# Kernel optimization log

Measured on AMD Instinct MI355X. Metric: run time of the kernel, lower is better.

The kernel has to match this reference:

```python
import jax, jax.numpy as jnp
import numpy as np

B, N, C = 4, 4096, 2048
EPS = 1e-5  # torch.nn.LayerNorm default


def setup_inputs() -> dict:
    key = jax.random.key(0)
    kx, = jax.random.split(key, 1)
    x = jax.random.normal(kx, (B, N, C), dtype=jnp.float32)
    gamma = jnp.ones((C,), dtype=jnp.float32)   # LayerNorm weight
    beta = jnp.zeros((C,), dtype=jnp.float32)   # LayerNorm bias
    return {"x": x, "gamma": gamma, "beta": beta}


def reference(x, gamma, beta):
    # The original repeats x to (B,N,N,C), applies a (no-op on the diagonal)
    # triu mask, FFTs every row over C, and extracts the (n,n) diagonal.
    # The diagonal rows are exactly the unmasked originals, so this equals:
    #   LayerNorm(real(fft(x, axis=-1)))
    y = jnp.fft.fft(x, axis=-1).real  # (B,N,C)
    mu = jnp.mean(y, axis=-1, keepdims=True)
    var = jnp.mean(jnp.square(y - mu), axis=-1, keepdims=True)  # biased, as torch LN
    return (y - mu) * jax.lax.rsqrt(var + EPS) * gamma + beta
```

## Files before the change

kernel.cpp:

```cpp
#include <hip/hip_runtime.h>
#include <math.h>


#define TPB 256
#define CD  2048

__device__ __forceinline__ float2 cadd(float2 a, float2 b){ return make_float2(a.x+b.x, a.y+b.y); }
__device__ __forceinline__ float2 csub(float2 a, float2 b){ return make_float2(a.x-b.x, a.y-b.y); }

__device__ __forceinline__ void dft8(const float2* z, float2* y)
{
    const float C8 = 0.70710678118654752440f;
    float2 a0=cadd(z[0],z[4]), a1=cadd(z[1],z[5]), a2=cadd(z[2],z[6]), a3=cadd(z[3],z[7]);
    float2 b0=csub(z[0],z[4]), b1=csub(z[1],z[5]), b2=csub(z[2],z[6]), b3=csub(z[3],z[7]);
    float2 t1=make_float2(C8*(b1.x+b1.y), C8*(b1.y-b1.x));
    float2 t2=make_float2(b2.y, -b2.x);
    float2 t3=make_float2(C8*(b3.y-b3.x), -C8*(b3.x+b3.y));
    {
        float pr=a0.x+a2.x, pi=a0.y+a2.y, mr=a0.x-a2.x, mi=a0.y-a2.y;
        float qr=a1.x+a3.x, qi=a1.y+a3.y, nr=a1.x-a3.x, ni=a1.y-a3.y;
        y[0]=make_float2(pr+qr,pi+qi); y[2]=make_float2(mr+ni,mi-nr);
        y[4]=make_float2(pr-qr,pi-qi); y[6]=make_float2(mr-ni,mi+nr);
    }
    {
        float pr=b0.x+t2.x, pi=b0.y+t2.y, mr=b0.x-t2.x, mi=b0.y-t2.y;
        float qr=t1.x+t3.x, qi=t1.y+t3.y, nr=t1.x-t3.x, ni=t1.y-t3.y;
        y[1]=make_float2(pr+qr,pi+qi); y[3]=make_float2(mr+ni,mi-nr);
        y[5]=make_float2(pr-qr,pi-qi); y[7]=make_float2(mr-ni,mi+nr);
    }
}

template<int S_, int OFFM>
__device__ __forceinline__ void r8_store(float2* Lw, const float2* y, int p)
{
    Lw[0] = y[0];
    if (S_ == 64 && p == 0) {
#pragma unroll
        for (int r = 1; r < 8; ++r) Lw[OFFM*r] = y[r];
        return;
    }
    const float th = -6.28318530717958647692f * ((float)S_ / 2048.0f);
    float s1, c1;
    __sincosf(th * (float)p, &s1, &c1);
    const float c2 = c1*c1 - s1*s1, s2 = 2.0f*c1*s1;
    const float c4 = c2*c2 - s2*s2, s4 = 2.0f*c2*s2;
    const float c3 = c1*c2 - s1*s2, s3 = s1*c2 + c1*s2;
    const float c5 = c1*c4 - s1*s4, s5 = s1*c4 + c1*s4;
    const float c6 = c2*c4 - s2*s4, s6 = s2*c4 + c2*s4;
    const float c7 = c3*c4 - s3*s4, s7 = s3*c4 + c3*s4;
    const float cw[8] = {1.f, c1, c2, c3, c4, c5, c6, c7};
    const float sw[8] = {0.f, s1, s2, s3, s4, s5, s6, s7};
#pragma unroll
    for (int r = 1; r < 8; ++r)
        Lw[OFFM*r] = make_float2(cw[r]*y[r].x - sw[r]*y[r].y,
                                 cw[r]*y[r].y + sw[r]*y[r].x);
}

__global__ __launch_bounds__(TPB, 8) void fourier_ln_kernel(
    const float* __restrict__ x,
    const float* __restrict__ gamma,
    const float* __restrict__ beta,
    float* __restrict__ out)
{
    __shared__ float2 L[2304];
    __shared__ float rmem[16];

    const int t  = threadIdx.x;
    const int t8 = t >> 3;
    const long long row0 = 2LL * (long long)blockIdx.x;
    const float* __restrict__ x0 = x + row0 * CD;
    const float* __restrict__ x1 = x0 + CD;

    float2 z[8], y[8];
#pragma unroll
    for (int r = 0; r < 8; ++r) {
        const int k = t + 256*r;
        z[r] = make_float2(x0[k], x1[k]);
    }

    float2* const Lr = L + (t + t8);

    dft8(z, y);
    r8_store<1, 1>(L + 9*t, y, t);
    __syncthreads();
#pragma unroll
    for (int r = 0; r < 8; ++r) z[r] = Lr[288*r];
    __syncthreads();

    dft8(z, y);
    r8_store<8, 9>(L + ((t & 7) + 72*t8), y, t8);
    __syncthreads();
#pragma unroll
    for (int r = 0; r < 8; ++r) z[r] = Lr[288*r];
    __syncthreads();

    dft8(z, y);
    {
        const int q = t & 63, p = t >> 6;
        r8_store<64, 72>(L + (q + (q >> 3) + 576*p), y, p);
    }
    __syncthreads();

    const int u   = t >> 1;
    const int sig = (t & 1) ? ((u == 0) ? 128 : 256 - u) : u;

    {
        const float2* Lsig = L + (sig + (sig >> 3));
#pragma unroll
        for (int r = 0; r < 8; ++r) z[r] = Lsig[288*r];
    }

    float gv[8], bv[8];
#pragma unroll
    for (int j = 0; j < 8; ++j) {
        gv[j] = gamma[sig + 256*j];
        bv[j] = beta[sig + 256*j];
    }

    float2 Z[8];
    {
        float pr=z[0].x+z[4].x, pi=z[0].y+z[4].y, mr=z[0].x-z[4].x, mi=z[0].y-z[4].y;
        float qr=z[2].x+z[6].x, qi=z[2].y+z[6].y, nr=z[2].x-z[6].x, ni=z[2].y-z[6].y;
        Z[0]=make_float2(pr+qr,pi+qi); Z[2]=make_float2(mr+ni,mi-nr);
        Z[4]=make_float2(pr-qr,pi-qi); Z[6]=make_float2(mr-ni,mi+nr);
    }
    {
        float pr=z[1].x+z[5].x, pi=z[1].y+z[5].y, mr=z[1].x-z[5].x, mi=z[1].y-z[5].y;
        float qr=z[3].x+z[7].x, qi=z[3].y+z[7].y, nr=z[3].x-z[7].x, ni=z[3].y-z[7].y;
        Z[1]=make_float2(pr+qr,pi+qi); Z[3]=make_float2(mr+ni,mi-nr);
        Z[5]=make_float2(pr-qr,pi-qi); Z[7]=make_float2(mr-ni,mi+nr);
    }

    float y0v[8], y1v[8];
    float s0=0.f, ss0=0.f, s1=0.f, ss1=0.f;
#pragma unroll
    for (int j = 0; j < 8; ++j) {
        float vx = __shfl_xor(Z[7-j].x, 1, 64);
        float vy = __shfl_xor(Z[7-j].y, 1, 64);
        const int ja = (8-j) & 7;
        float ax = (t == 0) ? Z[ja].x : Z[7-j].x;
        float ay = (t == 0) ? Z[ja].y : Z[7-j].y;
        vx = (t < 2) ? ax : vx;
        vy = (t < 2) ? ay : vy;
        float a = 0.5f*(Z[j].x + vx);
        float b = 0.5f*(Z[j].y + vy);
        y0v[j]=a; y1v[j]=b;
        s0+=a; ss0+=a*a; s1+=b; ss1+=b*b;
    }

#pragma unroll
    for (int off = 32; off > 0; off >>= 1) {
        s0  += __shfl_down(s0,  off, 64);
        ss0 += __shfl_down(ss0, off, 64);
        s1  += __shfl_down(s1,  off, 64);
        ss1 += __shfl_down(ss1, off, 64);
    }
    const int wave = t >> 6;
    if ((t & 63) == 0) {
        rmem[4*wave+0]=s0; rmem[4*wave+1]=ss0; rmem[4*wave+2]=s1; rmem[4*wave+3]=ss1;
    }
    __syncthreads();
    float S0=0.f, SS0=0.f, S1=0.f, SS1=0.f;
#pragma unroll
    for (int w = 0; w < 4; ++w) {
        S0+=rmem[4*w+0]; SS0+=rmem[4*w+1]; S1+=rmem[4*w+2]; SS1+=rmem[4*w+3];
    }
    const float inv = 1.0f/(float)CD;
    const float mu0 = S0*inv, mu1 = S1*inv;
    const float r0 = rsqrtf(SS0*inv - mu0*mu0 + 1e-5f);
    const float r1 = rsqrtf(SS1*inv - mu1*mu1 + 1e-5f);

    float* __restrict__ o0 = out + row0*CD;
    float* __restrict__ o1 = o0 + CD;
#pragma unroll
    for (int j = 0; j < 8; ++j) {
        const int k = sig + 256*j;
        const float rg0 = r0 * gv[j], rg1 = r1 * gv[j];
        o0[k] = (y0v[j] - mu0) * rg0 + bv[j];
        o1[k] = (y1v[j] - mu1) * rg1 + bv[j];
    }
}

extern "C" void kernel_launch(void* const* d_in, const int* in_sizes, int n_in,
                              void* d_out, int out_size, void* d_ws, size_t ws_size,
                              hipStream_t stream) {
    (void)in_sizes; (void)n_in; (void)d_ws; (void)ws_size; (void)out_size;
    const float* x     = (const float*)d_in[0];
    const float* gamma = (const float*)d_in[1];
    const float* beta  = (const float*)d_in[2];
    float* out = (float*)d_out;

    const int total_rows = 4 * 4096;
    const int blocks = total_rows / 2;
    fourier_ln_kernel<<<blocks, TPB, 0, stream>>>(x, gamma, beta, out);
}
```

Before: 236.9 us.

## Process four rows per block sharing twiddles and barriers across two FFT pairs

Each block now handles two packed complex row pairs (four real rows) with separate shared buffers, computing twiddle factors once per stage and reusing them for both pairs. This halves the number of barriers and twiddle sincos evaluations per row and gives more independent work between syncs. In exchange it doubles shared memory and register use per block and lowers the launch-bounds occupancy hint from 8 to 4 blocks, and halves the grid size.

```diff
diff --git a/kernel.cpp b/kernel.cpp
--- a/kernel.cpp
+++ b/kernel.cpp
@@ -30,93 +30,34 @@
     }
 }
 
-template<int S_, int OFFM>
-__device__ __forceinline__ void r8_store(float2* Lw, const float2* y, int p)
+__device__ __forceinline__ void make_tw(float th1, float* cw, float* sw)
+{
+    float s1, c1;
+    __sincosf(th1, &s1, &c1);
+    cw[0]=1.f;                       sw[0]=0.f;
+    cw[1]=c1;                        sw[1]=s1;
+    cw[2]=c1*c1-s1*s1;               sw[2]=2.f*c1*s1;
+    cw[4]=cw[2]*cw[2]-sw[2]*sw[2];   sw[4]=2.f*cw[2]*sw[2];
+    cw[3]=c1*cw[2]-s1*sw[2];         sw[3]=s1*cw[2]+c1*sw[2];
+    cw[5]=c1*cw[4]-s1*sw[4];         sw[5]=s1*cw[4]+c1*sw[4];
+    cw[6]=cw[2]*cw[4]-sw[2]*sw[4];   sw[6]=sw[2]*cw[4]+cw[2]*sw[4];
+    cw[7]=cw[3]*cw[4]-sw[3]*sw[4];   sw[7]=sw[3]*cw[4]+cw[3]*sw[4];
+}
+
+template<int OFFM>
+__device__ __forceinline__ void r8_store(float2* Lw, const float2* y,
+                                         const float* cw, const float* sw)
 {
     Lw[0] = y[0];
-    if (S_ == 64 && p == 0) {
-#pragma unroll
-        for (int r = 1; r < 8; ++r) Lw[OFFM*r] = y[r];
-        return;
-    }
-    const float th = -6.28318530717958647692f * ((float)S_ / 2048.0f);
-    float s1, c1;
-    __sincosf(th * (float)p, &s1, &c1);
-    const float c2 = c1*c1 - s1*s1, s2 = 2.0f*c1*s1;
-    const float c4 = c2*c2 - s2*s2, s4 = 2.0f*c2*s2;
-    const float c3 = c1*c2 - s1*s2, s3 = s1*c2 + c1*s2;
-    const float c5 = c1*c4 - s1*s4, s5 = s1*c4 + c1*s4;
-    const float c6 = c2*c4 - s2*s4, s6 = s2*c4 + c2*s4;
-    const float c7 = c3*c4 - s3*s4, s7 = s3*c4 + c3*s4;
-    const float cw[8] = {1.f, c1, c2, c3, c4, c5, c6, c7};
-    const float sw[8] = {0.f, s1, s2, s3, s4, s5, s6, s7};
 #pragma unroll
     for (int r = 1; r < 8; ++r)
         Lw[OFFM*r] = make_float2(cw[r]*y[r].x - sw[r]*y[r].y,
                                  cw[r]*y[r].y + sw[r]*y[r].x);
 }
 
-__global__ __launch_bounds__(TPB, 8) void fourier_ln_kernel(
-    const float* __restrict__ x,
-    const float* __restrict__ gamma,
-    const float* __restrict__ beta,
-    float* __restrict__ out)
-{
-    __shared__ float2 L[2304];
-    __shared__ float rmem[16];
-
-    const int t  = threadIdx.x;
-    const int t8 = t >> 3;
-    const long long row0 = 2LL * (long long)blockIdx.x;
-    const float* __restrict__ x0 = x + row0 * CD;
-    const float* __restrict__ x1 = x0 + CD;
-
-    float2 z[8], y[8];
-#pragma unroll
-    for (int r = 0; r < 8; ++r) {
-        const int k = t + 256*r;
-        z[r] = make_float2(x0[k], x1[k]);
-    }
-
-    float2* const Lr = L + (t + t8);
-
-    dft8(z, y);
-    r8_store<1, 1>(L + 9*t, y, t);
-    __syncthreads();
-#pragma unroll
-    for (int r = 0; r < 8; ++r) z[r] = Lr[288*r];
-    __syncthreads();
-
-    dft8(z, y);
-    r8_store<8, 9>(L + ((t & 7) + 72*t8), y, t8);
-    __syncthreads();
-#pragma unroll
-    for (int r = 0; r < 8; ++r) z[r] = Lr[288*r];
-    __syncthreads();
-
-    dft8(z, y);
-    {
-        const int q = t & 63, p = t >> 6;
-        r8_store<64, 72>(L + (q + (q >> 3) + 576*p), y, p);
-    }
-    __syncthreads();
-
-    const int u   = t >> 1;
-    const int sig = (t & 1) ? ((u == 0) ? 128 : 256 - u) : u;
-
-    {
-        const float2* Lsig = L + (sig + (sig >> 3));
-#pragma unroll
-        for (int r = 0; r < 8; ++r) z[r] = Lsig[288*r];
-    }
-
-    float gv[8], bv[8];
-#pragma unroll
-    for (int j = 0; j < 8; ++j) {
-        gv[j] = gamma[sig + 256*j];
-        bv[j] = beta[sig + 256*j];
-    }
-
+__device__ __forceinline__ void stageD_untangle(const float2* z, int t,
+        float* y0v, float* y1v, float& s0, float& ss0, float& s1, float& ss1)
+{
     float2 Z[8];
     {
         float pr=z[0].x+z[4].x, pi=z[0].y+z[4].y, mr=z[0].x-z[4].x, mi=z[0].y-z[4].y;
@@ -130,9 +71,6 @@
         Z[1]=make_float2(pr+qr,pi+qi); Z[3]=make_float2(mr+ni,mi-nr);
         Z[5]=make_float2(pr-qr,pi-qi); Z[7]=make_float2(mr-ni,mi+nr);
     }
-
-    float y0v[8], y1v[8];
-    float s0=0.f, ss0=0.f, s1=0.f, ss1=0.f;
 #pragma unroll
     for (int j = 0; j < 8; ++j) {
         float vx = __shfl_xor(Z[7-j].x, 1, 64);
@@ -147,37 +85,137 @@
         y0v[j]=a; y1v[j]=b;
         s0+=a; ss0+=a*a; s1+=b; ss1+=b*b;
     }
+}
+
+__global__ __launch_bounds__(TPB, 4) void fourier_ln_kernel(
+    const float* __restrict__ x,
+    const float* __restrict__ gamma,
+    const float* __restrict__ beta,
+    float* __restrict__ out)
+{
+    __shared__ float2 LA[2304];
+    __shared__ float2 LB[2304];
+    __shared__ float rmem[32];
+
+    const int t  = threadIdx.x;
+    const int t8 = t >> 3;
+    const long long rowa = 4LL * (long long)blockIdx.x;
+    const float* __restrict__ xa0 = x + rowa * CD;
+    const float* __restrict__ xa1 = xa0 + CD;
+    const float* __restrict__ xb0 = xa0 + 2 * CD;
+    const float* __restrict__ xb1 = xa0 + 3 * CD;
+
+    float2 za[8], zb[8], y[8];
+#pragma unroll
+    for (int r = 0; r < 8; ++r) {
+        const int k = t + 256*r;
+        za[r] = make_float2(xa0[k], xa1[k]);
+    }
+#pragma unroll
+    for (int r = 0; r < 8; ++r) {
+        const int k = t + 256*r;
+        zb[r] = make_float2(xb0[k], xb1[k]);
+    }
+
+    float2* const LAr = LA + (t + t8);
+    float2* const LBr = LB + (t + t8);
+
+    float cw[8], sw[8];
+
+    make_tw(-3.06796157577128245943e-3f * (float)t, cw, sw);
+    dft8(za, y);  r8_store<1>(LA + 9*t, y, cw, sw);
+    dft8(zb, y);  r8_store<1>(LB + 9*t, y, cw, sw);
+    __syncthreads();
+#pragma unroll
+    for (int r = 0; r < 8; ++r) za[r] = LAr[288*r];
+#pragma unroll
+    for (int r = 0; r < 8; ++r) zb[r] = LBr[288*r];
+    __syncthreads();
+
+    make_tw(-2.45436926061702596755e-2f * (float)t8, cw, sw);
+    dft8(za, y);  r8_store<9>(LA + ((t & 7) + 72*t8), y, cw, sw);
+    dft8(zb, y);  r8_store<9>(LB + ((t & 7) + 72*t8), y, cw, sw);
+    __syncthreads();
+#pragma unroll
+    for (int r = 0; r < 8; ++r) za[r] = LAr[288*r];
+#pragma unroll
+    for (int r = 0; r < 8; ++r) zb[r] = LBr[288*r];
+    __syncthreads();
+
+    {
+        const int q = t & 63, p = t >> 6;
+        make_tw(-1.96349540849362077404e-1f * (float)p, cw, sw);
+        const int off = q + (q >> 3) + 576*p;
+        dft8(za, y);  r8_store<72>(LA + off, y, cw, sw);
+        dft8(zb, y);  r8_store<72>(LB + off, y, cw, sw);
+    }
+    __syncthreads();
+
+    const int u   = t >> 1;
+    const int sig = (t & 1) ? ((u == 0) ? 128 : 256 - u) : u;
+
+    {
+        const int soff = sig + (sig >> 3);
+        const float2* LAs = LA + soff;
+        const float2* LBs = LB + soff;
+#pragma unroll
+        for (int r = 0; r < 8; ++r) za[r] = LAs[288*r];
+#pragma unroll
+        for (int r = 0; r < 8; ++r) zb[r] = LBs[288*r];
+    }
+
+    float gv[8], bv[8];
+#pragma unroll
+    for (int j = 0; j < 8; ++j) {
+        gv[j] = gamma[sig + 256*j];
+        bv[j] = beta[sig + 256*j];
+    }
+
+    float y0a[8], y1a[8], y0b[8], y1b[8];
+    float sa0=0.f, ssa0=0.f, sa1=0.f, ssa1=0.f;
+    float sb0=0.f, ssb0=0.f, sb1=0.f, ssb1=0.f;
+    stageD_untangle(za, t, y0a, y1a, sa0, ssa0, sa1, ssa1);
+    stageD_untangle(zb, t, y0b, y1b, sb0, ssb0, sb1, ssb1);
 
 #pragma unroll
     for (int off = 32; off > 0; off >>= 1) {
-        s0  += __shfl_down(s0,  off, 64);
-        ss0 += __shfl_down(ss0, off, 64);
-        s1  += __shfl_down(s1,  off, 64);
-        ss1 += __shfl_down(ss1, off, 64);
+        sa0 += __shfl_down(sa0, off, 64);  ssa0 += __shfl_down(ssa0, off, 64);
+        sa1 += __shfl_down(sa1, off, 64);  ssa1 += __shfl_down(ssa1, off, 64);
+        sb0 += __shfl_down(sb0, off, 64);  ssb0 += __shfl_down(ssb0, off, 64);
+        sb1 += __shfl_down(sb1, off, 64);  ssb1 += __shfl_down(ssb1, off, 64);
     }
     const int wave = t >> 6;
     if ((t & 63) == 0) {
-        rmem[4*wave+0]=s0; rmem[4*wave+1]=ss0; rmem[4*wave+2]=s1; rmem[4*wave+3]=ss1;
-    }
-    __syncthreads();
-    float S0=0.f, SS0=0.f, S1=0.f, SS1=0.f;
+        rmem[8*wave+0]=sa0; rmem[8*wave+1]=ssa0; rmem[8*wave+2]=sa1; rmem[8*wave+3]=ssa1;
+        rmem[8*wave+4]=sb0; rmem[8*wave+5]=ssb0; rmem[8*wave+6]=sb1; rmem[8*wave+7]=ssb1;
+    }
+    __syncthreads();
+    float SA0=0.f, SSA0=0.f, SA1=0.f, SSA1=0.f;
+    float SB0=0.f, SSB0=0.f, SB1=0.f, SSB1=0.f;
 #pragma unroll
     for (int w = 0; w < 4; ++w) {
-        S0+=rmem[4*w+0]; SS0+=rmem[4*w+1]; S1+=rmem[4*w+2]; SS1+=rmem[4*w+3];
+        SA0+=rmem[8*w+0]; SSA0+=rmem[8*w+1]; SA1+=rmem[8*w+2]; SSA1+=rmem[8*w+3];
+        SB0+=rmem[8*w+4]; SSB0+=rmem[8*w+5]; SB1+=rmem[8*w+6]; SSB1+=rmem[8*w+7];
     }
     const float inv = 1.0f/(float)CD;
-    const float mu0 = S0*inv, mu1 = S1*inv;
-    const float r0 = rsqrtf(SS0*inv - mu0*mu0 + 1e-5f);
-    const float r1 = rsqrtf(SS1*inv - mu1*mu1 + 1e-5f);
-
-    float* __restrict__ o0 = out + row0*CD;
-    float* __restrict__ o1 = o0 + CD;
+    const float mua0 = SA0*inv, mua1 = SA1*inv, mub0 = SB0*inv, mub1 = SB1*inv;
+    const float ra0 = rsqrtf(SSA0*inv - mua0*mua0 + 1e-5f);
+    const float ra1 = rsqrtf(SSA1*inv - mua1*mua1 + 1e-5f);
+    const float rb0 = rsqrtf(SSB0*inv - mub0*mub0 + 1e-5f);
+    const float rb1 = rsqrtf(SSB1*inv - mub1*mub1 + 1e-5f);
+
+    float* __restrict__ oa0 = out + rowa*CD;
+    float* __restrict__ oa1 = oa0 + CD;
+    float* __restrict__ ob0 = oa0 + 2*CD;
+    float* __restrict__ ob1 = oa0 + 3*CD;
 #pragma unroll
     for (int j = 0; j < 8; ++j) {
         const int k = sig + 256*j;
-        const float rg0 = r0 * gv[j], rg1 = r1 * gv[j];
-        o0[k] = (y0v[j] - mu0) * rg0 + bv[j];
-        o1[k] = (y1v[j] - mu1) * rg1 + bv[j];
+        const float g = gv[j], be = bv[j];
+        oa0[k] = (y0a[j] - mua0) * ra0 * g + be;
+        oa1[k] = (y1a[j] - mua1) * ra1 * g + be;
+        ob0[k] = (y0b[j] - mub0) * rb0 * g + be;
+        ob1[k] = (y1b[j] - mub1) * rb1 * g + be;
     }
 }
 
@@ -191,6 +229,6 @@
     float* out = (float*)d_out;
 
     const int total_rows = 4 * 4096;
-    const int blocks = total_rows / 2;
+    const int blocks = total_rows / 4;
     fourier_ln_kernel<<<blocks, TPB, 0, stream>>>(x, gamma, beta, out);
 }
```

Result: no change. 236.1 us (-0.4%).

## Stage LN outputs in LDS for float4 coalesced stores and vector gamma/beta loads

Applied to the files above, without the earlier changes.

Before normalisation, the post-processed spectrum values are written back into shared memory. The final pass then reads them contiguously and writes each output row with float4 stores, where it previously used scattered scalar stores indexed by sig. Gamma and beta are now loaded as float4 after the reduction barrier. Twiddle generation is moved into a separate helper, and the p==0 special case in the last stage is removed. The cost is extra LDS traffic and a dependence on the padded LDS layout lining up with contiguous output indices.

```diff
diff --git a/kernel.cpp b/kernel.cpp
--- a/kernel.cpp
+++ b/kernel.cpp
@@ -30,26 +30,25 @@
     }
 }
 
-template<int S_, int OFFM>
-__device__ __forceinline__ void r8_store(float2* Lw, const float2* y, int p)
+__device__ __forceinline__ void make_tw(float th1, float* cw, float* sw)
+{
+    float s1, c1;
+    __sincosf(th1, &s1, &c1);
+    cw[0]=1.f;                       sw[0]=0.f;
+    cw[1]=c1;                        sw[1]=s1;
+    cw[2]=c1*c1-s1*s1;               sw[2]=2.f*c1*s1;
+    cw[4]=cw[2]*cw[2]-sw[2]*sw[2];   sw[4]=2.f*cw[2]*sw[2];
+    cw[3]=c1*cw[2]-s1*sw[2];         sw[3]=s1*cw[2]+c1*sw[2];
+    cw[5]=c1*cw[4]-s1*sw[4];         sw[5]=s1*cw[4]+c1*sw[4];
+    cw[6]=cw[2]*cw[4]-sw[2]*sw[4];   sw[6]=sw[2]*cw[4]+cw[2]*sw[4];
+    cw[7]=cw[3]*cw[4]-sw[3]*sw[4];   sw[7]=sw[3]*cw[4]+cw[3]*sw[4];
+}
+
+template<int OFFM>
+__device__ __forceinline__ void r8_store(float2* Lw, const float2* y,
+                                         const float* cw, const float* sw)
 {
     Lw[0] = y[0];
-    if (S_ == 64 && p == 0) {
-#pragma unroll
-        for (int r = 1; r < 8; ++r) Lw[OFFM*r] = y[r];
-        return;
-    }
-    const float th = -6.28318530717958647692f * ((float)S_ / 2048.0f);
-    float s1, c1;
-    __sincosf(th * (float)p, &s1, &c1);
-    const float c2 = c1*c1 - s1*s1, s2 = 2.0f*c1*s1;
-    const float c4 = c2*c2 - s2*s2, s4 = 2.0f*c2*s2;
-    const float c3 = c1*c2 - s1*s2, s3 = s1*c2 + c1*s2;
-    const float c5 = c1*c4 - s1*s4, s5 = s1*c4 + c1*s4;
-    const float c6 = c2*c4 - s2*s4, s6 = s2*c4 + c2*s4;
-    const float c7 = c3*c4 - s3*s4, s7 = s3*c4 + c3*s4;
-    const float cw[8] = {1.f, c1, c2, c3, c4, c5, c6, c7};
-    const float sw[8] = {0.f, s1, s2, s3, s4, s5, s6, s7};
 #pragma unroll
     for (int r = 1; r < 8; ++r)
         Lw[OFFM*r] = make_float2(cw[r]*y[r].x - sw[r]*y[r].y,
@@ -79,16 +78,19 @@
     }
 
     float2* const Lr = L + (t + t8);
-
+    float cw[8], sw[8];
+
+    make_tw(-3.06796157577128245943e-3f * (float)t, cw, sw);
     dft8(z, y);
-    r8_store<1, 1>(L + 9*t, y, t);
+    r8_store<1>(L + 9*t, y, cw, sw);
     __syncthreads();
 #pragma unroll
     for (int r = 0; r < 8; ++r) z[r] = Lr[288*r];
     __syncthreads();
 
+    make_tw(-2.45436926061702596755e-2f * (float)t8, cw, sw);
     dft8(z, y);
-    r8_store<8, 9>(L + ((t & 7) + 72*t8), y, t8);
+    r8_store<9>(L + ((t & 7) + 72*t8), y, cw, sw);
     __syncthreads();
 #pragma unroll
     for (int r = 0; r < 8; ++r) z[r] = Lr[288*r];
@@ -97,25 +99,17 @@
     dft8(z, y);
     {
         const int q = t & 63, p = t >> 6;
-        r8_store<64, 72>(L + (q + (q >> 3) + 576*p), y, p);
+        make_tw(-1.96349540849362077404e-1f * (float)p, cw, sw);
+        r8_store<72>(L + (q + (q >> 3) + 576*p), y, cw, sw);
     }
     __syncthreads();
 
     const int u   = t >> 1;
     const int sig = (t & 1) ? ((u == 0) ? 128 : 256 - u) : u;
 
-    {
-        const float2* Lsig = L + (sig + (sig >> 3));
-#pragma unroll
-        for (int r = 0; r < 8; ++r) z[r] = Lsig[288*r];
-    }
-
-    float gv[8], bv[8];
-#pragma unroll
-    for (int j = 0; j < 8; ++j) {
-        gv[j] = gamma[sig + 256*j];
-        bv[j] = beta[sig + 256*j];
-    }
+    float2* const Lsig = L + (sig + (sig >> 3));
+#pragma unroll
+    for (int r = 0; r < 8; ++r) z[r] = Lsig[288*r];
 
     float2 Z[8];
     {
@@ -131,7 +125,6 @@
         Z[5]=make_float2(pr-qr,pi-qi); Z[7]=make_float2(mr-ni,mi+nr);
     }
 
-    float y0v[8], y1v[8];
     float s0=0.f, ss0=0.f, s1=0.f, ss1=0.f;
 #pragma unroll
     for (int j = 0; j < 8; ++j) {
@@ -144,7 +137,7 @@
         vy = (t < 2) ? ay : vy;
         float a = 0.5f*(Z[j].x + vx);
         float b = 0.5f*(Z[j].y + vy);
-        y0v[j]=a; y1v[j]=b;
+        Lsig[288*j] = make_float2(a, b);
         s0+=a; ss0+=a*a; s1+=b; ss1+=b*b;
     }
 
@@ -160,6 +153,12 @@
         rmem[4*wave+0]=s0; rmem[4*wave+1]=ss0; rmem[4*wave+2]=s1; rmem[4*wave+3]=ss1;
     }
     __syncthreads();
+
+    const float4 g0 = ((const float4*)gamma)[t];
+    const float4 b0 = ((const float4*)beta )[t];
+    const float4 g1 = ((const float4*)gamma)[t + 256];
+    const float4 b1 = ((const float4*)beta )[t + 256];
+
     float S0=0.f, SS0=0.f, S1=0.f, SS1=0.f;
 #pragma unroll
     for (int w = 0; w < 4; ++w) {
@@ -170,14 +169,24 @@
     const float r0 = rsqrtf(SS0*inv - mu0*mu0 + 1e-5f);
     const float r1 = rsqrtf(SS1*inv - mu1*mu1 + 1e-5f);
 
-    float* __restrict__ o0 = out + row0*CD;
-    float* __restrict__ o1 = o0 + CD;
-#pragma unroll
-    for (int j = 0; j < 8; ++j) {
-        const int k = sig + 256*j;
-        const float rg0 = r0 * gv[j], rg1 = r1 * gv[j];
-        o0[k] = (y0v[j] - mu0) * rg0 + bv[j];
-        o1[k] = (y1v[j] - mu1) * rg1 + bv[j];
+    const float2* const Ls = L + (4*t + (t >> 1));
+    float4* __restrict__ o0 = (float4*)(out + row0*CD);
+    float4* __restrict__ o1 = (float4*)(out + (row0+1)*CD);
+#pragma unroll
+    for (int h = 0; h < 2; ++h) {
+        float2 p0 = Ls[1152*h + 0];
+        float2 p1 = Ls[1152*h + 1];
+        float2 p2 = Ls[1152*h + 2];
+        float2 p3 = Ls[1152*h + 3];
+        const float4 g = h ? g1 : g0;
+        const float4 be = h ? b1 : b0;
+        float4 v0, v1;
+        v0.x=(p0.x-mu0)*r0*g.x+be.x; v1.x=(p0.y-mu1)*r1*g.x+be.x;
+        v0.y=(p1.x-mu0)*r0*g.y+be.y; v1.y=(p1.y-mu1)*r1*g.y+be.y;
+        v0.z=(p2.x-mu0)*r0*g.z+be.z; v1.z=(p2.y-mu1)*r1*g.z+be.z;
+        v0.w=(p3.x-mu0)*r0*g.w+be.w; v1.w=(p3.y-mu1)*r1*g.w+be.w;
+        o0[t + 256*h] = v0;
+        o1[t + 256*h] = v1;
     }
 }
 
```

Measured after the change: 231.5 us. 2.3% less time.
